# Kernel optimization log

Measured on AMD Instinct MI355X. Metric: run time of the kernel, lower is better.

The kernel has to match this reference:

```python
import jax, jax.numpy as jnp
import numpy as np

N, D, T, P, NP, H = 200000, 128, 8, 2000, 9, 2048


def setup_inputs() -> dict:
    key = jax.random.key(0)
    ks = jax.random.split(key, 12)
    inp = {
        'motion_z': jax.random.normal(ks[0], (N, D), jnp.float32),
        'tasks': jax.random.randint(ks[1], (N,), 0, T, jnp.int32),
        'tasks_mask': jax.random.randint(ks[2], (N,), 0, 2, jnp.int32),
        'patient_ids': jax.random.randint(ks[3], (N,), 0, P, jnp.int32),
        'phenos': jax.random.uniform(ks[4], (N, NP), jnp.float32),
        'phenos_mask': jax.random.randint(ks[5], (N,), 0, 2, jnp.int32),
        'W1': jax.random.normal(ks[6], (T * D, H), jnp.float32) * 0.02,
        'b1': jnp.zeros((H,), jnp.float32),
        'W2': jax.random.normal(ks[7], (H, H), jnp.float32) * 0.02,
        'b2': jnp.zeros((H,), jnp.float32),
        'W3': jax.random.normal(ks[8], (H, NP), jnp.float32) * 0.02,
        'b3': jnp.zeros((NP,), jnp.float32),
    }
    return inp


def _fingerprint(motion_z, tasks, tasks_mask, patient_ids, phenos, phenos_mask):
    # valid sample mask (tasks_mask==1 & patient id present & phenos_mask==1)
    valid = (tasks_mask == 1) & (phenos_mask == 1)
    w = valid.astype(motion_z.dtype)                      # [N]
    wz = motion_z * w[:, None]                            # [N, D]

    # global per-task mean (fallback for empty patient-task cells)
    t_sum = jax.ops.segment_sum(wz, tasks, num_segments=T)           # [T, D]
    t_cnt = jax.ops.segment_sum(w, tasks, num_segments=T)            # [T]
    task_mean = t_sum / jnp.maximum(t_cnt, 1.0)[:, None]             # [T, D]

    # fused (patient, task) segment mean — single pass scatter-reduce
    seg = patient_ids * T + tasks                                    # [N]
    pt_sum = jax.ops.segment_sum(wz, seg, num_segments=P * T)        # [P*T, D]
    pt_cnt = jax.ops.segment_sum(w, seg, num_segments=P * T)         # [P*T]
    pt_mean = pt_sum / jnp.maximum(pt_cnt, 1.0)[:, None]
    pt_mean = jnp.where((pt_cnt > 0)[:, None], pt_mean,
                        jnp.tile(task_mean, (P, 1)))                 # fallback
    fingerprint = pt_mean.reshape(P, T * D)

    # first valid pheno row per patient (phenos_id_each[0])
    idxs = jnp.where(valid, jnp.arange(N), N)
    first = jnp.full((P,), N, jnp.int32).at[patient_ids].min(idxs.astype(jnp.int32))
    uni_phenos = phenos[jnp.clip(first, 0, N - 1)]                   # [P, NP]
    return fingerprint, uni_phenos


def reference(motion_z, tasks, tasks_mask, patient_ids, phenos, phenos_mask,
              W1, b1, W2, b2, W3, b3):
    fingerprint, uni_phenos = _fingerprint(
        motion_z, tasks, tasks_mask, patient_ids, phenos, phenos_mask)
    h = jax.nn.relu(fingerprint @ W1 + b1)
    h = jax.nn.relu(h @ W2 + b2)
    pheno_latent = h @ W3 + b3
    out = jax.nn.sigmoid(pheno_latent)
    return out, uni_phenos, pheno_latent
```

## Files before the change

### kernel.cpp

```cpp
#include <hip/hip_runtime.h>
#include <math.h>

#define N_SAMP 200000
#define D_     128
#define T_     8
#define P_     2000
#define NP_    9
#define H_     2048
#define MPAD   2048
#define NSEG   16000

#define OFF_PTSUM   0
#define OFF_CNT     8192000
#define OFF_TSUM    8256000
#define OFF_TCNT    8260096
#define OFF_FMAX    8260352
#define ZERO_BYTES  8268352
#define OFF_FPHI    8268544
#define OFF_FPLO    12462848
#define OFF_W1THI   16657152
#define OFF_W1TLO   20851456
#define OFF_H1HI    25045760
#define OFF_H1LO    33434368
#define OFF_W2THI   41822976
#define OFF_W2TLO   50211584
#define OFF_H2      OFF_FPHI

typedef __attribute__((ext_vector_type(8))) short bf16x8;
typedef __attribute__((ext_vector_type(4))) float f32x4;

__device__ __forceinline__ unsigned f2bf_rne(float x) {
    unsigned b = __float_as_uint(x);
    return (b + 0x7fffu + ((b >> 16) & 1u)) >> 16;
}
__device__ __forceinline__ float bf2f(unsigned u) {
    return __uint_as_float(u << 16);
}

__device__ __forceinline__ void gload16(const void* g, void* l) {
    __builtin_amdgcn_global_load_lds(
        (const __attribute__((address_space(1))) unsigned int*)g,
        (__attribute__((address_space(3))) unsigned int*)l, 16, 0, 0);
}

__global__ __launch_bounds__(256) void scatter_pt(
    const float* __restrict__ motion_z, const int* __restrict__ tasks,
    const int* __restrict__ tmask, const int* __restrict__ pids,
    const int* __restrict__ pmask, float* __restrict__ pt_sum,
    float* __restrict__ cnt, unsigned* __restrict__ fmax)
{
    __shared__ unsigned list[256];
    __shared__ int nvalid;
    int tid  = threadIdx.x;
    int lane = tid & 63;
    int wv   = tid >> 6;
    for (int base = blockIdx.x * 256; base < N_SAMP; base += gridDim.x * 256) {
        if (tid == 0) nvalid = 0;
        __syncthreads();
        int i = base + tid;
        if (i < N_SAMP && tmask[i] == 1 && pmask[i] == 1) {
            int p = pids[i];
            int seg = p * T_ + tasks[i];
            atomicAdd(&cnt[seg], 1.0f);
            atomicMax(&fmax[p], (unsigned)(N_SAMP - i));
            int pos = atomicAdd(&nvalid, 1);
            list[pos] = ((unsigned)seg << 18) | (unsigned)i;
        }
        __syncthreads();
        int nv = nvalid;
        for (int e = wv; e < nv; e += 4) {
            unsigned pk = list[e];
            int row = (int)(pk & 0x3FFFFu);
            int seg = (int)(pk >> 18);
            float2 v = *(const float2*)&motion_z[(size_t)row * D_ + lane * 2];
            atomicAdd(&pt_sum[seg * D_ + lane * 2 + 0], v.x);
            atomicAdd(&pt_sum[seg * D_ + lane * 2 + 1], v.y);
        }
        __syncthreads();
    }
}

__global__ __launch_bounds__(256) void mid_fused(
    const float* __restrict__ pt_sum, const float* __restrict__ cnt,
    float* __restrict__ tsum, float* __restrict__ tcnt,
    const float* __restrict__ W1, const float* __restrict__ W2,
    unsigned short* __restrict__ w1hi, unsigned short* __restrict__ w1lo,
    unsigned short* __restrict__ w2hi, unsigned short* __restrict__ w2lo)
{
    __shared__ float tile[32][33];
    int tid = threadIdx.x;
    if (blockIdx.x < 125) {
        int p0 = blockIdx.x * 16;
        float4 acc = make_float4(0.f, 0.f, 0.f, 0.f);
        for (int pl = 0; pl < 16; ++pl) {
            float4 v = *(const float4*)&pt_sum[(size_t)(p0 + pl) * 1024 + tid * 4];
            acc.x += v.x; acc.y += v.y; acc.z += v.z; acc.w += v.w;
        }
        atomicAdd(&tsum[tid * 4 + 0], acc.x);
        atomicAdd(&tsum[tid * 4 + 1], acc.y);
        atomicAdd(&tsum[tid * 4 + 2], acc.z);
        atomicAdd(&tsum[tid * 4 + 3], acc.w);
        if (tid < 128) {
            int p = p0 + (tid >> 3), t = tid & 7;
            atomicAdd(&tcnt[t], cnt[p * 8 + t]);
        }
        return;
    }
    int id = blockIdx.x - 125;
    const float* W; unsigned short *Whi, *Wlo; int K;
    if (id < 2048) { W = W1; Whi = w1hi; Wlo = w1lo; K = 1024; }
    else { id -= 2048; W = W2; Whi = w2hi; Wlo = w2lo; K = 2048; }
    int bx = id & 63, by = id >> 6;
    int k0 = by * 32, n0 = bx * 32;
    const int N = 2048;
    int r = tid >> 3, c4 = (tid & 7) * 4;
    float4 v = *(const float4*)&W[(size_t)(k0 + r) * N + n0 + c4];
    tile[r][c4 + 0] = v.x; tile[r][c4 + 1] = v.y;
    tile[r][c4 + 2] = v.z; tile[r][c4 + 3] = v.w;
    __syncthreads();
    unsigned short hi[4], lo[4];
#pragma unroll
    for (int q = 0; q < 4; ++q) {
        float x = tile[c4 + q][r];
        unsigned h = f2bf_rne(x);
        hi[q] = (unsigned short)h;
        lo[q] = (unsigned short)f2bf_rne(x - bf2f(h));
    }
    size_t o = (size_t)(n0 + r) * K + k0 + c4;
    *(ushort4*)&Whi[o] = make_ushort4(hi[0], hi[1], hi[2], hi[3]);
    *(ushort4*)&Wlo[o] = make_ushort4(lo[0], lo[1], lo[2], lo[3]);
}

__global__ __launch_bounds__(256) void finalize_fused(
    const float* __restrict__ pt_sum, const float* __restrict__ cnt,
    const float* __restrict__ tsum, const float* __restrict__ tcnt,
    const unsigned* __restrict__ fmax, const float* __restrict__ phenos,
    unsigned short* __restrict__ fphi, unsigned short* __restrict__ fplo,
    float* __restrict__ uni)
{
    if (blockIdx.x < 1024) {
        int e8 = blockIdx.x * 256 + threadIdx.x;
        int e  = e8 * 8;
        int p = e >> 10, col0 = e & 1023;
        int seg = p * T_ + (col0 >> 7);
        ushort hi[8], lo[8];
        if (p < P_) {
            float c = cnt[seg];
            float4 a = *(const float4*)&pt_sum[e];
            float4 b = *(const float4*)&pt_sum[e + 4];
            float vv[8] = {a.x, a.y, a.z, a.w, b.x, b.y, b.z, b.w};
#pragma unroll
            for (int q = 0; q < 8; ++q) {
                float v;
                if (c > 0.f) v = vv[q] / c;
                else         v = tsum[col0 + q] / fmaxf(tcnt[col0 >> 7], 1.0f);
                unsigned h = f2bf_rne(v);
                hi[q] = (ushort)h;
                lo[q] = (ushort)f2bf_rne(v - bf2f(h));
            }
        } else {
#pragma unroll
            for (int q = 0; q < 8; ++q) { hi[q] = 0; lo[q] = 0; }
        }
        *(ushort4*)&fphi[e]     = make_ushort4(hi[0], hi[1], hi[2], hi[3]);
        *(ushort4*)&fphi[e + 4] = make_ushort4(hi[4], hi[5], hi[6], hi[7]);
        *(ushort4*)&fplo[e]     = make_ushort4(lo[0], lo[1], lo[2], lo[3]);
        *(ushort4*)&fplo[e + 4] = make_ushort4(lo[4], lo[5], lo[6], lo[7]);
    } else {
        int g = (blockIdx.x - 1024) * 256 + threadIdx.x;
        if (g < P_ * NP_) {
            int p = g / NP_, j = g - p * NP_;
            unsigned fm = fmax[p];
            int idx = fm ? (int)(N_SAMP - fm) : N_SAMP - 1;
            uni[g] = phenos[(size_t)idx * NP_ + j];
        }
    }
}

template<int OUTF32>
__global__ __launch_bounds__(256, 1) void gemm_split(
    const unsigned short* __restrict__ Ahi, const unsigned short* __restrict__ Alo,
    const unsigned short* __restrict__ Bhi, const unsigned short* __restrict__ Blo,
    const float* __restrict__ bias,
    float* __restrict__ Cf, unsigned short* __restrict__ Chi,
    unsigned short* __restrict__ Clo, int K)
{
    __shared__ __align__(16) char lds[2][4][8192];
    int tid  = threadIdx.x;
    int lane = tid & 63, w = tid >> 6;
    int wr = w >> 1, wc = w & 1;
    int row0 = blockIdx.y * 128, col0 = blockIdx.x * 128;

    int fr = lane & 15;
    int fk = (lane >> 4) * 8;

    const unsigned short* srcs[4] = {Ahi, Alo, Bhi, Blo};
    int base0[4] = {row0, row0, col0, col0};

    auto STAGE = [&](int buf, int t) {
        int k0 = t * 32;
#pragma unroll
        for (int pc = 0; pc < 4; ++pc) {
#pragma unroll
            for (int rep = 0; rep < 2; ++rep) {
                int tile = rep * 4 + w;
                const unsigned short* g =
                    srcs[pc] + (size_t)(base0[pc] + tile * 16 + fr) * K + k0 + fk;
                gload16(g, &lds[buf][pc][tile * 1024]);
            }
        }
    };

    f32x4 acc[4][4] = {};
    int nt = K / 32;
    STAGE(0, 0);
    __syncthreads();
    int cur = 0;
    int lo16 = lane * 16;

    for (int t = 0; t < nt; ++t) {
        if (t + 1 < nt) STAGE(cur ^ 1, t + 1);
        bf16x8 ah[4], al[4], bh[4], bl[4];
#pragma unroll
        for (int i = 0; i < 4; ++i) {
            ah[i] = *(const bf16x8*)&lds[cur][0][(wr * 4 + i) * 1024 + lo16];
            al[i] = *(const bf16x8*)&lds[cur][1][(wr * 4 + i) * 1024 + lo16];
        }
#pragma unroll
        for (int j = 0; j < 4; ++j) {
            bh[j] = *(const bf16x8*)&lds[cur][2][(wc * 4 + j) * 1024 + lo16];
            bl[j] = *(const bf16x8*)&lds[cur][3][(wc * 4 + j) * 1024 + lo16];
        }
#pragma unroll
        for (int i = 0; i < 4; ++i)
#pragma unroll
            for (int j = 0; j < 4; ++j) {
                acc[i][j] = __builtin_amdgcn_mfma_f32_16x16x32_bf16(ah[i], bh[j], acc[i][j], 0, 0, 0);
                acc[i][j] = __builtin_amdgcn_mfma_f32_16x16x32_bf16(ah[i], bl[j], acc[i][j], 0, 0, 0);
                acc[i][j] = __builtin_amdgcn_mfma_f32_16x16x32_bf16(al[i], bh[j], acc[i][j], 0, 0, 0);
            }
        __syncthreads();
        cur ^= 1;
    }

#pragma unroll
    for (int i = 0; i < 4; ++i) {
        int r = row0 + wr * 64 + i * 16 + (lane >> 4) * 4;
#pragma unroll
        for (int j = 0; j < 4; ++j) {
            int c = col0 + wc * 64 + j * 16 + (lane & 15);
            float bv = bias[c];
#pragma unroll
            for (int q = 0; q < 4; ++q) {
                float x = fmaxf(acc[i][j][q] + bv, 0.f);
                size_t o = (size_t)(r + q) * H_ + c;
                if (OUTF32) {
                    Cf[o] = x;
                } else {
                    unsigned hb = f2bf_rne(x);
                    Chi[o] = (unsigned short)hb;
                    Clo[o] = (unsigned short)f2bf_rne(x - bf2f(hb));
                }
            }
        }
    }
}

__global__ __launch_bounds__(256) void out_head(
    const float* __restrict__ h2, const float* __restrict__ W3,
    const float* __restrict__ b3, float* __restrict__ out,
    float* __restrict__ latent)
{
    __shared__ float w3s[H_ * NP_];
    int tid = threadIdx.x;
    for (int e = tid * 4; e < H_ * NP_; e += 1024)
        *(float4*)&w3s[e] = *(const float4*)&W3[e];
    __syncthreads();

    int wid  = blockIdx.x * 4 + (tid >> 6);
    int lane = tid & 63;
    if (wid >= P_) return;
    const float* hrow = h2 + (size_t)wid * H_;
    float acc[NP_] = {};
    for (int k = lane; k < H_; k += 64) {
        float h = hrow[k];
#pragma unroll
        for (int j = 0; j < NP_; ++j) acc[j] = fmaf(h, w3s[k * NP_ + j], acc[j]);
    }
#pragma unroll
    for (int off = 32; off > 0; off >>= 1)
#pragma unroll
        for (int j = 0; j < NP_; ++j) acc[j] += __shfl_down(acc[j], off);
    if (lane == 0) {
#pragma unroll
        for (int j = 0; j < NP_; ++j) {
            float v = acc[j] + b3[j];
            latent[wid * NP_ + j] = v;
            out[wid * NP_ + j]    = 1.f / (1.f + expf(-v));
        }
    }
}

extern "C" void kernel_launch(void* const* d_in, const int* in_sizes, int n_in,
                              void* d_out, int out_size, void* d_ws, size_t ws_size,
                              hipStream_t stream)
{
    const float* motion_z = (const float*)d_in[0];
    const int*   tasks    = (const int*)d_in[1];
    const int*   tmask    = (const int*)d_in[2];
    const int*   pids     = (const int*)d_in[3];
    const float* phenos   = (const float*)d_in[4];
    const int*   pmask    = (const int*)d_in[5];
    const float* W1 = (const float*)d_in[6];
    const float* b1 = (const float*)d_in[7];
    const float* W2 = (const float*)d_in[8];
    const float* b2 = (const float*)d_in[9];
    const float* W3 = (const float*)d_in[10];
    const float* b3 = (const float*)d_in[11];

    char* ws = (char*)d_ws;
    float*          pt_sum = (float*)(ws + OFF_PTSUM);
    float*          cnt    = (float*)(ws + OFF_CNT);
    float*          tsum   = (float*)(ws + OFF_TSUM);
    float*          tcnt   = (float*)(ws + OFF_TCNT);
    unsigned*       fmax   = (unsigned*)(ws + OFF_FMAX);
    unsigned short* fphi   = (unsigned short*)(ws + OFF_FPHI);
    unsigned short* fplo   = (unsigned short*)(ws + OFF_FPLO);
    unsigned short* w1thi  = (unsigned short*)(ws + OFF_W1THI);
    unsigned short* w1tlo  = (unsigned short*)(ws + OFF_W1TLO);
    unsigned short* h1hi   = (unsigned short*)(ws + OFF_H1HI);
    unsigned short* h1lo   = (unsigned short*)(ws + OFF_H1LO);
    unsigned short* w2thi  = (unsigned short*)(ws + OFF_W2THI);
    unsigned short* w2tlo  = (unsigned short*)(ws + OFF_W2TLO);
    float*          h2     = (float*)(ws + OFF_H2);

    float* out    = (float*)d_out;
    float* uni    = out + P_ * NP_;
    float* latent = out + 2 * P_ * NP_;

    hipMemsetAsync(ws, 0, ZERO_BYTES, stream);

    scatter_pt<<<782, 256, 0, stream>>>(motion_z, tasks, tmask, pids, pmask,
                                        pt_sum, cnt, fmax);
    mid_fused<<<125 + 6144, 256, 0, stream>>>(pt_sum, cnt, tsum, tcnt,
                                              W1, W2, w1thi, w1tlo, w2thi, w2tlo);
    finalize_fused<<<1024 + (P_ * NP_ + 255) / 256, 256, 0, stream>>>(
        pt_sum, cnt, tsum, tcnt, fmax, phenos, fphi, fplo, uni);

    gemm_split<0><<<dim3(16, 16), 256, 0, stream>>>(
        fphi, fplo, w1thi, w1tlo, b1, nullptr, h1hi, h1lo, 1024);
    gemm_split<1><<<dim3(16, 16), 256, 0, stream>>>(
        h1hi, h1lo, w2thi, w2tlo, b2, h2, nullptr, nullptr, H_);

    out_head<<<P_ / 4, 256, 0, stream>>>(h2, W3, b3, out, latent);
}
```

Baseline: 420.8 us.

## Give each wave private LDS tiles and drop block barriers in split-bf16 GEMM

Each wave now loads into its own LDS region exactly the A and B tiles it consumes, rather than the block sharing tiles. Loads are prefetched two stages ahead and ordered with explicit vmcnt/lgkmcnt waits instead of __syncthreads. The aim is to remove block-wide barrier stalls and deepen the load pipeline. In exchange each tile is loaded by two waves, which doubles global and L2 traffic, and LDS use doubles to 128KB.

```diff
diff --git a/kernel.cpp b/kernel.cpp
--- a/kernel.cpp
+++ b/kernel.cpp
@@ -185,7 +185,7 @@
     float* __restrict__ Cf, unsigned short* __restrict__ Chi,
     unsigned short* __restrict__ Clo, int K)
 {
-    __shared__ __align__(16) char lds[2][4][8192];
+    __shared__ __align__(16) char lds[4][2][16384];
     int tid  = threadIdx.x;
     int lane = tid & 63, w = tid >> 6;
     int wr = w >> 1, wc = w & 1;
@@ -194,42 +194,44 @@
     int fr = lane & 15;
     int fk = (lane >> 4) * 8;
 
-    const unsigned short* srcs[4] = {Ahi, Alo, Bhi, Blo};
-    int base0[4] = {row0, row0, col0, col0};
+    const unsigned short* cbase[16];
+#pragma unroll
+    for (int c = 0; c < 16; ++c) {
+        int isB = c >> 3, i = (c >> 1) & 3, h = c & 1;
+        const unsigned short* src = isB ? (h ? Blo : Bhi) : (h ? Alo : Ahi);
+        int rb = (isB ? col0 + (wc * 4 + i) * 16 : row0 + (wr * 4 + i) * 16) + fr;
+        cbase[c] = src + (size_t)rb * K + fk;
+    }
+    char* wlds = &lds[w][0][0];
 
     auto STAGE = [&](int buf, int t) {
         int k0 = t * 32;
 #pragma unroll
-        for (int pc = 0; pc < 4; ++pc) {
-#pragma unroll
-            for (int rep = 0; rep < 2; ++rep) {
-                int tile = rep * 4 + w;
-                const unsigned short* g =
-                    srcs[pc] + (size_t)(base0[pc] + tile * 16 + fr) * K + k0 + fk;
-                gload16(g, &lds[buf][pc][tile * 1024]);
-            }
-        }
+        for (int c = 0; c < 16; ++c)
+            gload16(cbase[c] + k0, wlds + buf * 16384 + c * 1024);
     };
 
     f32x4 acc[4][4] = {};
     int nt = K / 32;
     STAGE(0, 0);
-    __syncthreads();
-    int cur = 0;
+    STAGE(1, 1);
     int lo16 = lane * 16;
 
     for (int t = 0; t < nt; ++t) {
-        if (t + 1 < nt) STAGE(cur ^ 1, t + 1);
+        int cur = t & 1;
+        if (t + 1 < nt) asm volatile("s_waitcnt vmcnt(16)" ::: "memory");
+        else            asm volatile("s_waitcnt vmcnt(0)"  ::: "memory");
+        const char* b = wlds + cur * 16384;
         bf16x8 ah[4], al[4], bh[4], bl[4];
 #pragma unroll
         for (int i = 0; i < 4; ++i) {
-            ah[i] = *(const bf16x8*)&lds[cur][0][(wr * 4 + i) * 1024 + lo16];
-            al[i] = *(const bf16x8*)&lds[cur][1][(wr * 4 + i) * 1024 + lo16];
+            ah[i] = *(const bf16x8*)(b + (i * 2 + 0) * 1024 + lo16);
+            al[i] = *(const bf16x8*)(b + (i * 2 + 1) * 1024 + lo16);
         }
 #pragma unroll
         for (int j = 0; j < 4; ++j) {
-            bh[j] = *(const bf16x8*)&lds[cur][2][(wc * 4 + j) * 1024 + lo16];
-            bl[j] = *(const bf16x8*)&lds[cur][3][(wc * 4 + j) * 1024 + lo16];
+            bh[j] = *(const bf16x8*)(b + (8 + j * 2 + 0) * 1024 + lo16);
+            bl[j] = *(const bf16x8*)(b + (8 + j * 2 + 1) * 1024 + lo16);
         }
 #pragma unroll
         for (int i = 0; i < 4; ++i)
@@ -239,8 +241,10 @@
                 acc[i][j] = __builtin_amdgcn_mfma_f32_16x16x32_bf16(ah[i], bl[j], acc[i][j], 0, 0, 0);
                 acc[i][j] = __builtin_amdgcn_mfma_f32_16x16x32_bf16(al[i], bh[j], acc[i][j], 0, 0, 0);
             }
-        __syncthreads();
-        cur ^= 1;
+        if (t + 2 < nt) {
+            asm volatile("s_waitcnt lgkmcnt(0)" ::: "memory");
+            STAGE(cur, t + 2);
+        }
     }
 
 #pragma unroll
```

New measurement: 470.1 us. 11.7% more time.
